# Optimization experiments

Hardware: AMD Instinct MI355X
Metric: run time of the kernel (lower is better)

The kernel has to match this reference:

```python
import jax, jax.numpy as jnp
import numpy as np

N = 50000
E = 1000000
FN = 16
FE = 8
H = 64
DH = 64
LN_EPS = 1e-5


def _layernorm(x, g, b):
    mu = jnp.mean(x, axis=-1, keepdims=True)
    var = jnp.var(x, axis=-1, keepdims=True)
    return (x - mu) * jax.lax.rsqrt(var + LN_EPS) * g + b


def setup_inputs() -> dict:
    key = jax.random.key(0)
    ks = jax.random.split(key, 24)

    def w(k, i, o):
        return jax.random.normal(k, (i, o), jnp.float32) / np.sqrt(i).astype(np.float32)

    inp = {}
    inp["x"] = jax.random.normal(ks[0], (N, FN), jnp.float32)
    inp["edge_index"] = jax.random.randint(ks[1], (2, E), 0, N, dtype=jnp.int32)
    inp["edge_attr"] = jax.random.normal(ks[2], (E, FE), jnp.float32)
    # layer 0 (in_dim = FN, residual is a Linear since FN != H)
    inp["l0_lin_w"] = w(ks[3], FE, FN); inp["l0_lin_b"] = jnp.zeros((FN,), jnp.float32)
    inp["l0_w1"] = w(ks[4], FN, H);    inp["l0_b1"] = jnp.zeros((H,), jnp.float32)
    inp["l0_w2"] = w(ks[5], H, H);     inp["l0_b2"] = jnp.zeros((H,), jnp.float32)
    inp["l0_ln_g"] = jnp.ones((H,), jnp.float32); inp["l0_ln_b"] = jnp.zeros((H,), jnp.float32)
    inp["l0_res_w"] = w(ks[6], FN, H); inp["l0_res_b"] = jnp.zeros((H,), jnp.float32)
    # layers 1, 2 (in_dim = H, residual = identity)
    for li, base in ((1, 7), (2, 11)):
        inp[f"l{li}_lin_w"] = w(ks[base], FE, H);   inp[f"l{li}_lin_b"] = jnp.zeros((H,), jnp.float32)
        inp[f"l{li}_w1"] = w(ks[base + 1], H, H);   inp[f"l{li}_b1"] = jnp.zeros((H,), jnp.float32)
        inp[f"l{li}_w2"] = w(ks[base + 2], H, H);   inp[f"l{li}_b2"] = jnp.zeros((H,), jnp.float32)
        inp[f"l{li}_ln_g"] = jnp.ones((H,), jnp.float32)
        inp[f"l{li}_ln_b"] = jnp.zeros((H,), jnp.float32)
    D_IN = 4 * H + FE
    inp["dec_w1"] = w(ks[20], D_IN, DH);    inp["dec_b1"] = jnp.zeros((DH,), jnp.float32)
    inp["dec_w2"] = w(ks[21], DH, DH // 2); inp["dec_b2"] = jnp.zeros((DH // 2,), jnp.float32)
    inp["dec_w3"] = w(ks[22], DH // 2, 1);  inp["dec_b3"] = jnp.zeros((1,), jnp.float32)
    return inp


def _block(x, src, dst, edge_attr, lin_w, lin_b, w1, b1, w2, b2, ln_g, ln_b, res):
    # GINEConv: message = ReLU(x_src + Lin(edge_attr)); sum-aggregate at dst; eps=0
    msg = jax.nn.relu(x[src] + edge_attr @ lin_w + lin_b)      # (E, D_in)
    aggr = jax.ops.segment_sum(msg, dst, num_segments=N)       # (N, D_in)
    h = jax.nn.relu((x + aggr) @ w1 + b1) @ w2 + b2            # GIN nn MLP -> (N, H)
    h = jax.nn.relu(h)                                         # dropout inactive (eval)
    return _layernorm(h + res, ln_g, ln_b)


def reference(x, edge_index, edge_attr,
              l0_lin_w, l0_lin_b, l0_w1, l0_b1, l0_w2, l0_b2, l0_ln_g, l0_ln_b, l0_res_w, l0_res_b,
              l1_lin_w, l1_lin_b, l1_w1, l1_b1, l1_w2, l1_b2, l1_ln_g, l1_ln_b,
              l2_lin_w, l2_lin_b, l2_w1, l2_b1, l2_w2, l2_b2, l2_ln_g, l2_ln_b,
              dec_w1, dec_b1, dec_w2, dec_b2, dec_w3, dec_b3):
    src, dst = edge_index[0], edge_index[1]
    h = _block(x, src, dst, edge_attr, l0_lin_w, l0_lin_b, l0_w1, l0_b1, l0_w2, l0_b2,
               l0_ln_g, l0_ln_b, x @ l0_res_w + l0_res_b)
    h = _block(h, src, dst, edge_attr, l1_lin_w, l1_lin_b, l1_w1, l1_b1, l1_w2, l1_b2,
               l1_ln_g, l1_ln_b, h)
    h = _block(h, src, dst, edge_attr, l2_lin_w, l2_lin_b, l2_w1, l2_b1, l2_w2, l2_b2,
               l2_ln_g, l2_ln_b, h)
    hs, hd = h[src], h[dst]                                    # (E, H) each
    z = jnp.concatenate([hs, hd, jnp.abs(hs - hd), hs * hd, edge_attr], axis=-1)  # (E, 4H+FE)
    z = jax.nn.relu(z @ dec_w1 + dec_b1)
    z = jax.nn.relu(z @ dec_w2 + dec_b2)
    return (z @ dec_w3 + dec_b3)[:, 0]                         # (E,)
```

## Files before the change

kernel.cpp:

```cpp
#include <hip/hip_runtime.h>

#define NN 50000
#define NE 1000000

constexpr float LN_EPS = 1e-5f;

typedef short bf16x8 __attribute__((ext_vector_type(8)));
typedef float f32x4 __attribute__((ext_vector_type(4)));
typedef uint uvec4 __attribute__((ext_vector_type(4)));
typedef uint uvec2 __attribute__((ext_vector_type(2)));

__device__ inline uint cvtpk(float a, float b) {
  uint r;
  asm("v_cvt_pk_bf16_f32 %0, %1, %2" : "=v"(r) : "v"(a), "v"(b));
  return r;
}
__device__ inline ushort cvt1(float a) {
  uint r;
  asm("v_cvt_pk_bf16_f32 %0, %1, %1" : "=v"(r) : "v"(a));
  return (ushort)r;
}
__device__ inline float bflo(uint u) { union { uint x; float f; } v; v.x = u << 16; return v.f; }
__device__ inline float bfhi(uint u) { union { uint x; float f; } v; v.x = u & 0xffff0000u; return v.f; }

__global__ __launch_bounds__(256) void hist_kernel(const int* __restrict__ ei,
                                                   int* __restrict__ cnt) {
  int e = blockIdx.x * 256 + threadIdx.x;
  if (e < NE) atomicAdd(&cnt[ei[NE + e]], 1);
}

__global__ __launch_bounds__(256) void scan1_kernel(const int* __restrict__ cnt,
                                                    int* __restrict__ off,
                                                    int* __restrict__ bsum) {
  __shared__ int sh[256];
  int t = threadIdx.x;
  int idx = blockIdx.x * 256 + t;
  int v = (idx < NN) ? cnt[idx] : 0;
  sh[t] = v;
  __syncthreads();
  for (int o = 1; o < 256; o <<= 1) {
    int xv = (t >= o) ? sh[t - o] : 0;
    __syncthreads();
    sh[t] += xv;
    __syncthreads();
  }
  if (idx <= NN) off[idx] = sh[t] - v;
  if (t == 255) bsum[blockIdx.x] = sh[255];
}

__global__ __launch_bounds__(256) void scan2_kernel(int* __restrict__ bsum, int nb) {
  __shared__ int sh[256];
  int t = threadIdx.x;
  int v = (t < nb) ? bsum[t] : 0;
  sh[t] = v;
  __syncthreads();
  for (int o = 1; o < 256; o <<= 1) {
    int xv = (t >= o) ? sh[t - o] : 0;
    __syncthreads();
    sh[t] += xv;
    __syncthreads();
  }
  if (t < nb) bsum[t] = sh[t] - v;
}

__global__ __launch_bounds__(256) void scan3_kernel(int* __restrict__ off,
                                                    const int* __restrict__ bsum,
                                                    int* __restrict__ cnt) {
  int idx = blockIdx.x * 256 + threadIdx.x;
  if (idx <= NN) off[idx] += bsum[blockIdx.x];
  if (idx < NN) cnt[idx] = 0;
}

__global__ __launch_bounds__(256) void scatter_kernel(
    const int* __restrict__ ei, const float* __restrict__ ea,
    const int* __restrict__ off, int* __restrict__ cur,
    int* __restrict__ ipos, int* __restrict__ srcp, int* __restrict__ dstp,
    ushort* __restrict__ eapb) {
  int e = blockIdx.x * 256 + threadIdx.x;
  if (e < NE) {
    int d = ei[NE + e];
    int s = ei[e];
    int p = off[d] + atomicAdd(&cur[d], 1);
    ipos[e] = p;
    srcp[p] = s;
    dstp[p] = d;
    const float* eaf = ea + (size_t)e * 8;
    f32x4 e0 = *(const f32x4*)(eaf);
    f32x4 e1 = *(const f32x4*)(eaf + 4);
    uvec4 u;
    u.x = cvtpk(e0.x, e0.y);
    u.y = cvtpk(e0.z, e0.w);
    u.z = cvtpk(e1.x, e1.y);
    u.w = cvtpk(e1.z, e1.w);
    __builtin_nontemporal_store(u, (uvec4*)(eapb + (size_t)p * 8));
  }
}

__global__ __launch_bounds__(256) void unperm_kernel(const float* __restrict__ tmp,
                                                     const int* __restrict__ ipos,
                                                     float* __restrict__ out) {
  int e = blockIdx.x * 256 + threadIdx.x;
  if (e < NE) out[e] = tmp[ipos[e]];
}

__device__ inline float lane_layernorm(float r, float g, float b) {
  float s = r;
#pragma unroll
  for (int m = 32; m >= 1; m >>= 1) s += __shfl_xor(s, m);
  float mu = s * (1.f / 64.f);
  float dv = r - mu;
  float v = dv * dv;
#pragma unroll
  for (int m = 32; m >= 1; m >>= 1) v += __shfl_xor(v, m);
  float var = v * (1.f / 64.f);
  return dv * rsqrtf(var + LN_EPS) * g + b;
}

__global__ __launch_bounds__(256) void layer0_fused(
    const float* __restrict__ x, float* __restrict__ hout,
    ushort* __restrict__ houtbf,
    const ushort* __restrict__ eapb, const int* __restrict__ srcp,
    const int* __restrict__ off,
    const float* __restrict__ lw, const float* __restrict__ lb,
    const float* __restrict__ w1, const float* __restrict__ b1,
    const float* __restrict__ w2, const float* __restrict__ b2,
    const float* __restrict__ lng, const float* __restrict__ lnb,
    const float* __restrict__ rw, const float* __restrict__ rb) {
  int n = blockIdx.x * 4 + (threadIdx.x >> 6);
  int j = threadIdx.x & 63;
  int d = j & 15, slot = j >> 4;
  int start = off[n], end = off[n + 1];
  float lwv[8];
#pragma unroll
  for (int i = 0; i < 8; i++) lwv[i] = lw[i * 16 + d];
  float lbv = lb[d];
  float acc = 0.f;
  for (int base = start; base < end; base += 64) {
    int idx = base + j;
    int sl = (idx < end) ? srcp[idx] : 0;
    int c = min(end - base, 64);
    for (int i0 = 0; i0 < c; i0 += 4) {
      int i = i0 + slot;
      bool valid = i < c;
      int ii = i & 63;
      int s = __shfl(sl, ii);
      int pp = min(base + i0 + slot, NE - 1);
      float ev = bflo((uint)eapb[(size_t)pp * 8 + (d & 7)]);
      float xs = x[(size_t)s * 16 + d];
      float m = lbv + xs;
#pragma unroll
      for (int q = 0; q < 8; q++) m = fmaf(__shfl(ev, slot * 16 + q), lwv[q], m);
      m = fmaxf(m, 0.f);
      acc += valid ? m : 0.f;
    }
  }
  acc += __shfl_xor(acc, 16);
  acc += __shfl_xor(acc, 32);
  float xr = x[(size_t)n * 16 + d];
  float t = xr + acc;
  float q1 = b1[j];
#pragma unroll 4
  for (int k = 0; k < 16; k++) q1 = fmaf(__shfl(t, k), w1[k * 64 + j], q1);
  q1 = fmaxf(q1, 0.f);
  float h2 = b2[j];
  for (int k = 0; k < 64; k++) h2 = fmaf(__shfl(q1, k), w2[k * 64 + j], h2);
  h2 = fmaxf(h2, 0.f);
  float res = rb[j];
#pragma unroll 4
  for (int k = 0; k < 16; k++) res = fmaf(__shfl(xr, k), rw[k * 64 + j], res);
  float v = lane_layernorm(h2 + res, lng[j], lnb[j]);
  hout[(size_t)n * 64 + j] = v;
  houtbf[(size_t)n * 64 + j] = cvt1(v);
}

__device__ inline float edge8_msg(const ushort* __restrict__ hinb, int s, int j,
                                  uint ulo, uint uhi, uint vlo, uint vhi,
                                  const float* lwv, float lbv) {
  float hc = bflo((uint)hinb[(size_t)s * 64 + j]);
  float m = lbv + hc;
  m = fmaf(bflo(ulo), lwv[0], m);
  m = fmaf(bfhi(ulo), lwv[1], m);
  m = fmaf(bflo(uhi), lwv[2], m);
  m = fmaf(bfhi(uhi), lwv[3], m);
  m = fmaf(bflo(vlo), lwv[4], m);
  m = fmaf(bfhi(vlo), lwv[5], m);
  m = fmaf(bflo(vhi), lwv[6], m);
  m = fmaf(bfhi(vhi), lwv[7], m);
  return fmaxf(m, 0.f);
}

__global__ __launch_bounds__(256) void layer_fused(
    const ushort* __restrict__ hinb, const float* __restrict__ hinf,
    float* __restrict__ houtf, ushort* __restrict__ houtbf,
    const ushort* __restrict__ eapb, const int* __restrict__ srcp,
    const int* __restrict__ off,
    const float* __restrict__ lw, const float* __restrict__ lb,
    const float* __restrict__ w1, const float* __restrict__ b1,
    const float* __restrict__ w2, const float* __restrict__ b2,
    const float* __restrict__ lng, const float* __restrict__ lnb) {
  int n = blockIdx.x * 4 + (threadIdx.x >> 6);
  int j = threadIdx.x & 63;
  int start = __builtin_amdgcn_readfirstlane(off[n]);
  int end = __builtin_amdgcn_readfirstlane(off[n + 1]);
  float lwv[8];
#pragma unroll
  for (int i = 0; i < 8; i++) lwv[i] = lw[i * 64 + j];
  float lbv = lb[j];
  float acc = 0.f;
  int p = start;
  for (; p + 8 <= end; p += 8) {
    const uvec4* ip = (const uvec4*)(srcp + p);
    uvec4 I0 = __builtin_nontemporal_load(ip + 0);
    uvec4 I1 = __builtin_nontemporal_load(ip + 1);
    int s0 = __builtin_amdgcn_readfirstlane((int)I0.x);
    int s1 = __builtin_amdgcn_readfirstlane((int)I0.y);
    int s2 = __builtin_amdgcn_readfirstlane((int)I0.z);
    int s3 = __builtin_amdgcn_readfirstlane((int)I0.w);
    int s4 = __builtin_amdgcn_readfirstlane((int)I1.x);
    int s5 = __builtin_amdgcn_readfirstlane((int)I1.y);
    int s6 = __builtin_amdgcn_readfirstlane((int)I1.z);
    int s7 = __builtin_amdgcn_readfirstlane((int)I1.w);
    const uvec4* ep = (const uvec4*)(eapb + (size_t)p * 8);
    uint ua[8][4];
#pragma unroll
    for (int i = 0; i < 8; i++) {
      uvec4 E = __builtin_nontemporal_load(ep + i);
      ua[i][0] = __builtin_amdgcn_readfirstlane(E.x);
      ua[i][1] = __builtin_amdgcn_readfirstlane(E.y);
      ua[i][2] = __builtin_amdgcn_readfirstlane(E.z);
      ua[i][3] = __builtin_amdgcn_readfirstlane(E.w);
    }
    acc += edge8_msg(hinb, s0, j, ua[0][0], ua[0][1], ua[0][2], ua[0][3], lwv, lbv);
    acc += edge8_msg(hinb, s1, j, ua[1][0], ua[1][1], ua[1][2], ua[1][3], lwv, lbv);
    acc += edge8_msg(hinb, s2, j, ua[2][0], ua[2][1], ua[2][2], ua[2][3], lwv, lbv);
    acc += edge8_msg(hinb, s3, j, ua[3][0], ua[3][1], ua[3][2], ua[3][3], lwv, lbv);
    acc += edge8_msg(hinb, s4, j, ua[4][0], ua[4][1], ua[4][2], ua[4][3], lwv, lbv);
    acc += edge8_msg(hinb, s5, j, ua[5][0], ua[5][1], ua[5][2], ua[5][3], lwv, lbv);
    acc += edge8_msg(hinb, s6, j, ua[6][0], ua[6][1], ua[6][2], ua[6][3], lwv, lbv);
    acc += edge8_msg(hinb, s7, j, ua[7][0], ua[7][1], ua[7][2], ua[7][3], lwv, lbv);
  }
  for (; p < end; p++) {
    int s = __builtin_amdgcn_readfirstlane(srcp[p]);
    uvec4 E = __builtin_nontemporal_load((const uvec4*)(eapb + (size_t)p * 8));
    uint e0 = __builtin_amdgcn_readfirstlane(E.x);
    uint e1 = __builtin_amdgcn_readfirstlane(E.y);
    uint e2 = __builtin_amdgcn_readfirstlane(E.z);
    uint e3 = __builtin_amdgcn_readfirstlane(E.w);
    acc += edge8_msg(hinb, s, j, e0, e1, e2, e3, lwv, lbv);
  }
  float hv = __builtin_nontemporal_load(&hinf[(size_t)n * 64 + j]);
  float t = hv + acc;
  float q1 = b1[j];
  for (int k = 0; k < 64; k++) q1 = fmaf(__shfl(t, k), w1[k * 64 + j], q1);
  q1 = fmaxf(q1, 0.f);
  float h2 = b2[j];
  for (int k = 0; k < 64; k++) h2 = fmaf(__shfl(q1, k), w2[k * 64 + j], h2);
  h2 = fmaxf(h2, 0.f);
  float v = lane_layernorm(h2 + hv, lng[j], lnb[j]);
  if (houtf) houtf[(size_t)n * 64 + j] = v;
  houtbf[(size_t)n * 64 + j] = cvt1(v);
}

__global__ __launch_bounds__(256) void prep_kernel(
    const float* __restrict__ w1, const float* __restrict__ w2,
    ushort* __restrict__ w1f, ushort* __restrict__ w2f) {
  int t = blockIdx.x * 256 + threadIdx.x;
  if (t < 18432) {
    int j = t & 7, lane = (t >> 3) & 63, f = t >> 9;
    int k = (f >> 2) * 32 + ((lane >> 4) * 8) + j;
    int n = (f & 3) * 16 + (lane & 15);
    float v = (k < 264) ? w1[k * 64 + n] : 0.f;
    w1f[t] = cvt1(v);
  } else {
    int t2 = t - 18432;
    int j = t2 & 7, lane = (t2 >> 3) & 63, f = t2 >> 9;
    int k = (f >> 1) * 32 + ((lane >> 4) * 8) + j;
    int n = (f & 1) * 16 + (lane & 15);
    w2f[t2] = cvt1(w2[k * 32 + n]);
  }
}

#define YS 72
#define NGRP 31250
#define NBLK 15625
#define BPX 1954

__device__ inline ushort* zsw(ushort* Z, int row, int bo) {
  return (ushort*)((char*)Z + (((row << 9) + bo) ^ ((row & 7) << 4)));
}

__global__ __launch_bounds__(128, 2) void decoder_kernel(
    const ushort* __restrict__ hb,
    const int* __restrict__ srcp, const int* __restrict__ dstp,
    const ushort* __restrict__ eapb,
    const ushort* __restrict__ w1f, const ushort* __restrict__ w2f,
    const float* __restrict__ b1, const float* __restrict__ b2,
    const float* __restrict__ w3, const float* __restrict__ b3,
    float* __restrict__ tmp) {
  __shared__ ushort zbuf[2][32 * 256];
  const int w = threadIdx.x >> 6, l = threadIdx.x & 63;
  const int sub = l & 15, quad = l >> 4;
  int bb = (blockIdx.x & 7) * BPX + (blockIdx.x >> 3);
  if (bb >= NBLK) return;
  const int g = bb * 2 + w;
  ushort* Z = zbuf[w];
  ushort* Y = Z;

  int s32 = __builtin_nontemporal_load(&srcp[g * 32 + (l & 31)]);
  int d32 = __builtin_nontemporal_load(&dstp[g * 32 + (l & 31)]);
  uvec2 pa[8], pb[8];
#pragma unroll
  for (int i = 0; i < 8; i++) {
    int e = 4 * i + quad;
    int s = __shfl(s32, e), d = __shfl(d32, e);
    pa[i] = *(const uvec2*)&hb[(size_t)s * 64 + sub * 4];
    pb[i] = *(const uvec2*)&hb[(size_t)d * 64 + sub * 4];
  }
  bf16x8 eaA = (bf16x8){0, 0, 0, 0, 0, 0, 0, 0};
  bf16x8 eaB = (bf16x8){0, 0, 0, 0, 0, 0, 0, 0};
  if (quad == 0) {
    eaA = *(const bf16x8*)&eapb[((size_t)g * 32 + sub) * 8];
    eaB = *(const bf16x8*)&eapb[((size_t)g * 32 + 16 + sub) * 8];
  }

  float b1v[4];
#pragma unroll
  for (int t = 0; t < 4; t++) b1v[t] = b1[t * 16 + sub];
  float b2v0 = b2[sub], b2v1 = b2[16 + sub];
  float w3v0 = w3[sub], w3v1 = w3[16 + sub];
  float b3v = b3[0];

#pragma unroll
  for (int i = 0; i < 8; i++) {
    int e = 4 * i + quad;
    uvec2 a = pa[i], b = pb[i];
    *(uvec2*)zsw(Z, e, sub * 8) = a;
    *(uvec2*)zsw(Z, e, 128 + sub * 8) = b;
    float a0 = bflo(a.x), a1 = bfhi(a.x), a2 = bflo(a.y), a3 = bfhi(a.y);
    float c0 = bflo(b.x), c1 = bfhi(b.x), c2 = bflo(b.y), c3 = bfhi(b.y);
    uvec2 u;
    u.x = cvtpk(fabsf(a0 - c0), fabsf(a1 - c1));
    u.y = cvtpk(fabsf(a2 - c2), fabsf(a3 - c3));
    *(uvec2*)zsw(Z, e, 256 + sub * 8) = u;
    u.x = cvtpk(a0 * c0, a1 * c1);
    u.y = cvtpk(a2 * c2, a3 * c3);
    *(uvec2*)zsw(Z, e, 384 + sub * 8) = u;
  }

  f32x4 acc[2][4];
#pragma unroll
  for (int m = 0; m < 2; m++)
#pragma unroll
    for (int t = 0; t < 4; t++) acc[m][t] = (f32x4){0.f, 0.f, 0.f, 0.f};
#pragma unroll
  for (int s = 0; s < 8; s++) {
    bf16x8 afA = *(const bf16x8*)zsw(Z, sub, s * 64 + quad * 16);
    bf16x8 afB = *(const bf16x8*)zsw(Z, 16 + sub, s * 64 + quad * 16);
#pragma unroll
    for (int t = 0; t < 4; t++) {
      bf16x8 bf = ((const bf16x8*)w1f)[(s * 4 + t) * 64 + l];
      acc[0][t] = __builtin_amdgcn_mfma_f32_16x16x32_bf16(afA, bf, acc[0][t], 0, 0, 0);
      acc[1][t] = __builtin_amdgcn_mfma_f32_16x16x32_bf16(afB, bf, acc[1][t], 0, 0, 0);
    }
  }
#pragma unroll
  for (int t = 0; t < 4; t++) {
    bf16x8 bf = ((const bf16x8*)w1f)[(32 + t) * 64 + l];
    acc[0][t] = __builtin_amdgcn_mfma_f32_16x16x32_bf16(eaA, bf, acc[0][t], 0, 0, 0);
    acc[1][t] = __builtin_amdgcn_mfma_f32_16x16x32_bf16(eaB, bf, acc[1][t], 0, 0, 0);
  }
#pragma unroll
  for (int m = 0; m < 2; m++)
#pragma unroll
    for (int t = 0; t < 4; t++)
#pragma unroll
      for (int r = 0; r < 4; r++)
        Y[(m * 16 + quad * 4 + r) * YS + t * 16 + sub] =
            cvt1(fmaxf(acc[m][t][r] + b1v[t], 0.f));

  bf16x8 w2frag[4];
#pragma unroll
  for (int f = 0; f < 4; f++) w2frag[f] = ((const bf16x8*)w2f)[f * 64 + l];
  f32x4 acc2[2][2];
#pragma unroll
  for (int m = 0; m < 2; m++) {
    acc2[m][0] = (f32x4){0.f, 0.f, 0.f, 0.f};
    acc2[m][1] = (f32x4){0.f, 0.f, 0.f, 0.f};
#pragma unroll
    for (int ks = 0; ks < 2; ks++) {
      union { bf16x8 v; ushort4 u[2]; } ya;
      int o = (m * 16 + sub) * YS + ks * 32 + quad * 8;
      ya.u[0] = *(const ushort4*)&Y[o];
      ya.u[1] = *(const ushort4*)&Y[o + 4];
      acc2[m][0] = __builtin_amdgcn_mfma_f32_16x16x32_bf16(ya.v, w2frag[ks * 2 + 0],
                                                           acc2[m][0], 0, 0, 0);
      acc2[m][1] = __builtin_amdgcn_mfma_f32_16x16x32_bf16(ya.v, w2frag[ks * 2 + 1],
                                                           acc2[m][1], 0, 0, 0);
    }
  }
#pragma unroll
  for (int m = 0; m < 2; m++)
#pragma unroll
    for (int r = 0; r < 4; r++) {
      float o = fmaxf(acc2[m][0][r] + b2v0, 0.f) * w3v0 +
                fmaxf(acc2[m][1][r] + b2v1, 0.f) * w3v1;
      o += __shfl_xor(o, 1);
      o += __shfl_xor(o, 2);
      o += __shfl_xor(o, 4);
      o += __shfl_xor(o, 8);
      if (sub == 0) tmp[g * 32 + m * 16 + quad * 4 + r] = o + b3v;
    }
}

extern "C" void kernel_launch(void* const* d_in, const int* in_sizes, int n_in,
                              void* d_out, int out_size, void* d_ws, size_t ws_size,
                              hipStream_t stream) {
  const float* x = (const float*)d_in[0];
  const int* ei = (const int*)d_in[1];
  const float* ea = (const float*)d_in[2];
  const float* l0_lin_w = (const float*)d_in[3];
  const float* l0_lin_b = (const float*)d_in[4];
  const float* l0_w1 = (const float*)d_in[5];
  const float* l0_b1 = (const float*)d_in[6];
  const float* l0_w2 = (const float*)d_in[7];
  const float* l0_b2 = (const float*)d_in[8];
  const float* l0_ln_g = (const float*)d_in[9];
  const float* l0_ln_b = (const float*)d_in[10];
  const float* l0_res_w = (const float*)d_in[11];
  const float* l0_res_b = (const float*)d_in[12];
  const float* dec_w1 = (const float*)d_in[29];
  const float* dec_b1 = (const float*)d_in[30];
  const float* dec_w2 = (const float*)d_in[31];
  const float* dec_b2 = (const float*)d_in[32];
  const float* dec_w3 = (const float*)d_in[33];
  const float* dec_b3 = (const float*)d_in[34];

  float* h_a = (float*)d_ws;
  float* h_b = h_a + (size_t)NN * 64;
  ushort* hbA = (ushort*)(h_b + (size_t)NN * 64);
  ushort* hbB = hbA + (size_t)NN * 64;
  int* ipos = (int*)(hbB + (size_t)NN * 64);
  int* srcp = ipos + NE;
  int* dstp = srcp + NE;
  float* tmp = (float*)(dstp + NE);
  int* off = (int*)(tmp + NE);
  int* cnt = off + (NN + 1);
  int* bsum = cnt + NN;
  ushort* w1f = (ushort*)(bsum + 256);
  ushort* w2f = w1f + 18432;
  ushort* eapb = w2f + 2048;

  const int EB = (NE + 255) / 256;
  const int SB = (NN + 256) / 256;

  hipMemsetAsync(cnt, 0, (size_t)NN * sizeof(int), stream);
  hist_kernel<<<EB, 256, 0, stream>>>(ei, cnt);
  scan1_kernel<<<SB, 256, 0, stream>>>(cnt, off, bsum);
  scan2_kernel<<<1, 256, 0, stream>>>(bsum, SB);
  scan3_kernel<<<SB, 256, 0, stream>>>(off, bsum, cnt);
  scatter_kernel<<<EB, 256, 0, stream>>>(ei, ea, off, cnt, ipos, srcp, dstp, eapb);

  layer0_fused<<<NN / 4, 256, 0, stream>>>(x, h_a, hbA, eapb, srcp, off,
                                           l0_lin_w, l0_lin_b, l0_w1, l0_b1,
                                           l0_w2, l0_b2, l0_ln_g, l0_ln_b,
                                           l0_res_w, l0_res_b);
  layer_fused<<<NN / 4, 256, 0, stream>>>(hbA, h_a, h_b, hbB, eapb, srcp, off,
                                          (const float*)d_in[13], (const float*)d_in[14],
                                          (const float*)d_in[15], (const float*)d_in[16],
                                          (const float*)d_in[17], (const float*)d_in[18],
                                          (const float*)d_in[19], (const float*)d_in[20]);
  layer_fused<<<NN / 4, 256, 0, stream>>>(hbB, h_b, (float*)nullptr, hbA, eapb, srcp, off,
                                          (const float*)d_in[21], (const float*)d_in[22],
                                          (const float*)d_in[23], (const float*)d_in[24],
                                          (const float*)d_in[25], (const float*)d_in[26],
                                          (const float*)d_in[27], (const float*)d_in[28]);

  prep_kernel<<<80, 256, 0, stream>>>(dec_w1, dec_w2, w1f, w2f);
  decoder_kernel<<<8 * BPX, 128, 0, stream>>>(hbA, srcp, dstp, eapb,
                                              w1f, w2f, dec_b1, dec_b2,
                                              dec_w3, dec_b3, tmp);
  unperm_kernel<<<EB, 256, 0, stream>>>(tmp, ipos, (float*)d_out);
}
```

Baseline: 641.5 us.

## Load decoder MFMA A-fragments directly from gathered rows, drop LDS staging

The decoder previously gathered node embeddings into a swizzled 32x256 LDS tile, built the |a-b| and a*b features there, and then read MFMA A-fragments back from it. It now gathers each edge's src/dst rows straight into the MFMA A-fragment register layout (two 8-element chunks per lane) and computes the abs-diff and product fragments in registers. The K blocks are reordered to match, which removes the LDS writes and reads for the first layer. LDS shrinks to the small Y buffer, so launch bounds rise to 4 blocks per SM, and the Y read becomes a single 16-byte load. Register pressure grows, which could limit the extra occupancy.

```diff
diff --git a/kernel.cpp b/kernel.cpp
--- a/kernel.cpp
+++ b/kernel.cpp
@@ -281,15 +281,23 @@
 }
 
 #define YS 72
-#define NGRP 31250
 #define NBLK 15625
 #define BPX 1954
 
-__device__ inline ushort* zsw(ushort* Z, int row, int bo) {
-  return (ushort*)((char*)Z + (((row << 9) + bo) ^ ((row & 7) << 4)));
-}
-
-__global__ __launch_bounds__(128, 2) void decoder_kernel(
+__device__ inline void absmul(bf16x8 a, bf16x8 b, bf16x8& dd, bf16x8& pp) {
+  union U { bf16x8 v; uvec4 u; } ua, ub, ud, up;
+  ua.v = a; ub.v = b;
+#pragma unroll
+  for (int i = 0; i < 4; i++) {
+    float a0 = bflo(ua.u[i]), a1 = bfhi(ua.u[i]);
+    float b0 = bflo(ub.u[i]), b1 = bfhi(ub.u[i]);
+    ud.u[i] = cvtpk(fabsf(a0 - b0), fabsf(a1 - b1));
+    up.u[i] = cvtpk(a0 * b0, a1 * b1);
+  }
+  dd = ud.v; pp = up.v;
+}
+
+__global__ __launch_bounds__(128, 4) void decoder_kernel(
     const ushort* __restrict__ hb,
     const int* __restrict__ srcp, const int* __restrict__ dstp,
     const ushort* __restrict__ eapb,
@@ -297,30 +305,34 @@
     const float* __restrict__ b1, const float* __restrict__ b2,
     const float* __restrict__ w3, const float* __restrict__ b3,
     float* __restrict__ tmp) {
-  __shared__ ushort zbuf[2][32 * 256];
+  __shared__ ushort ybuf[2][32 * YS];
   const int w = threadIdx.x >> 6, l = threadIdx.x & 63;
   const int sub = l & 15, quad = l >> 4;
   int bb = (blockIdx.x & 7) * BPX + (blockIdx.x >> 3);
   if (bb >= NBLK) return;
   const int g = bb * 2 + w;
-  ushort* Z = zbuf[w];
-  ushort* Y = Z;
+  ushort* Y = ybuf[w];
 
   int s32 = __builtin_nontemporal_load(&srcp[g * 32 + (l & 31)]);
   int d32 = __builtin_nontemporal_load(&dstp[g * 32 + (l & 31)]);
-  uvec2 pa[8], pb[8];
-#pragma unroll
-  for (int i = 0; i < 8; i++) {
-    int e = 4 * i + quad;
-    int s = __shfl(s32, e), d = __shfl(d32, e);
-    pa[i] = *(const uvec2*)&hb[(size_t)s * 64 + sub * 4];
-    pb[i] = *(const uvec2*)&hb[(size_t)d * 64 + sub * 4];
-  }
-  bf16x8 eaA = (bf16x8){0, 0, 0, 0, 0, 0, 0, 0};
-  bf16x8 eaB = (bf16x8){0, 0, 0, 0, 0, 0, 0, 0};
+
+  bf16x8 alo[2], ahi[2], blo[2], bhi[2];
+#pragma unroll
+  for (int m = 0; m < 2; m++) {
+    int sA = __shfl(s32, m * 16 + sub);
+    int dA = __shfl(d32, m * 16 + sub);
+    const ushort* pa = hb + (size_t)sA * 64 + quad * 8;
+    const ushort* pb = hb + (size_t)dA * 64 + quad * 8;
+    alo[m] = *(const bf16x8*)pa;
+    ahi[m] = *(const bf16x8*)(pa + 32);
+    blo[m] = *(const bf16x8*)pb;
+    bhi[m] = *(const bf16x8*)(pb + 32);
+  }
+  bf16x8 eaf0 = (bf16x8){0, 0, 0, 0, 0, 0, 0, 0};
+  bf16x8 eaf1 = (bf16x8){0, 0, 0, 0, 0, 0, 0, 0};
   if (quad == 0) {
-    eaA = *(const bf16x8*)&eapb[((size_t)g * 32 + sub) * 8];
-    eaB = *(const bf16x8*)&eapb[((size_t)g * 32 + 16 + sub) * 8];
+    eaf0 = *(const bf16x8*)&eapb[((size_t)g * 32 + sub) * 8];
+    eaf1 = *(const bf16x8*)&eapb[((size_t)g * 32 + 16 + sub) * 8];
   }
 
   float b1v[4];
@@ -330,45 +342,44 @@
   float w3v0 = w3[sub], w3v1 = w3[16 + sub];
   float b3v = b3[0];
 
-#pragma unroll
-  for (int i = 0; i < 8; i++) {
-    int e = 4 * i + quad;
-    uvec2 a = pa[i], b = pb[i];
-    *(uvec2*)zsw(Z, e, sub * 8) = a;
-    *(uvec2*)zsw(Z, e, 128 + sub * 8) = b;
-    float a0 = bflo(a.x), a1 = bfhi(a.x), a2 = bflo(a.y), a3 = bfhi(a.y);
-    float c0 = bflo(b.x), c1 = bfhi(b.x), c2 = bflo(b.y), c3 = bfhi(b.y);
-    uvec2 u;
-    u.x = cvtpk(fabsf(a0 - c0), fabsf(a1 - c1));
-    u.y = cvtpk(fabsf(a2 - c2), fabsf(a3 - c3));
-    *(uvec2*)zsw(Z, e, 256 + sub * 8) = u;
-    u.x = cvtpk(a0 * c0, a1 * c1);
-    u.y = cvtpk(a2 * c2, a3 * c3);
-    *(uvec2*)zsw(Z, e, 384 + sub * 8) = u;
-  }
-
   f32x4 acc[2][4];
 #pragma unroll
   for (int m = 0; m < 2; m++)
 #pragma unroll
     for (int t = 0; t < 4; t++) acc[m][t] = (f32x4){0.f, 0.f, 0.f, 0.f};
-#pragma unroll
-  for (int s = 0; s < 8; s++) {
-    bf16x8 afA = *(const bf16x8*)zsw(Z, sub, s * 64 + quad * 16);
-    bf16x8 afB = *(const bf16x8*)zsw(Z, 16 + sub, s * 64 + quad * 16);
-#pragma unroll
-    for (int t = 0; t < 4; t++) {
-      bf16x8 bf = ((const bf16x8*)w1f)[(s * 4 + t) * 64 + l];
-      acc[0][t] = __builtin_amdgcn_mfma_f32_16x16x32_bf16(afA, bf, acc[0][t], 0, 0, 0);
-      acc[1][t] = __builtin_amdgcn_mfma_f32_16x16x32_bf16(afB, bf, acc[1][t], 0, 0, 0);
-    }
-  }
-#pragma unroll
-  for (int t = 0; t < 4; t++) {
-    bf16x8 bf = ((const bf16x8*)w1f)[(32 + t) * 64 + l];
-    acc[0][t] = __builtin_amdgcn_mfma_f32_16x16x32_bf16(eaA, bf, acc[0][t], 0, 0, 0);
-    acc[1][t] = __builtin_amdgcn_mfma_f32_16x16x32_bf16(eaB, bf, acc[1][t], 0, 0, 0);
-  }
+
+#define MF(sB, f0, f1)                                                        \
+  {                                                                           \
+    _Pragma("unroll") for (int t = 0; t < 4; t++) {                           \
+      bf16x8 bfv = ((const bf16x8*)w1f)[((sB)*4 + t) * 64 + l];               \
+      acc[0][t] = __builtin_amdgcn_mfma_f32_16x16x32_bf16(f0, bfv, acc[0][t], \
+                                                          0, 0, 0);           \
+      acc[1][t] = __builtin_amdgcn_mfma_f32_16x16x32_bf16(f1, bfv, acc[1][t], \
+                                                          0, 0, 0);           \
+    }                                                                         \
+  }
+
+  {
+    bf16x8 dlo0, plo0, dlo1, plo1;
+    absmul(alo[0], blo[0], dlo0, plo0);
+    absmul(alo[1], blo[1], dlo1, plo1);
+    MF(0, alo[0], alo[1]);
+    MF(2, blo[0], blo[1]);
+    MF(4, dlo0, dlo1);
+    MF(6, plo0, plo1);
+  }
+  {
+    bf16x8 dhi0, phi0, dhi1, phi1;
+    absmul(ahi[0], bhi[0], dhi0, phi0);
+    absmul(ahi[1], bhi[1], dhi1, phi1);
+    MF(1, ahi[0], ahi[1]);
+    MF(3, bhi[0], bhi[1]);
+    MF(5, dhi0, dhi1);
+    MF(7, phi0, phi1);
+  }
+  MF(8, eaf0, eaf1);
+#undef MF
+
 #pragma unroll
   for (int m = 0; m < 2; m++)
 #pragma unroll
@@ -388,13 +399,10 @@
     acc2[m][1] = (f32x4){0.f, 0.f, 0.f, 0.f};
 #pragma unroll
     for (int ks = 0; ks < 2; ks++) {
-      union { bf16x8 v; ushort4 u[2]; } ya;
-      int o = (m * 16 + sub) * YS + ks * 32 + quad * 8;
-      ya.u[0] = *(const ushort4*)&Y[o];
-      ya.u[1] = *(const ushort4*)&Y[o + 4];
-      acc2[m][0] = __builtin_amdgcn_mfma_f32_16x16x32_bf16(ya.v, w2frag[ks * 2 + 0],
+      bf16x8 ya = *(const bf16x8*)&Y[(m * 16 + sub) * YS + ks * 32 + quad * 8];
+      acc2[m][0] = __builtin_amdgcn_mfma_f32_16x16x32_bf16(ya, w2frag[ks * 2 + 0],
                                                            acc2[m][0], 0, 0, 0);
-      acc2[m][1] = __builtin_amdgcn_mfma_f32_16x16x32_bf16(ya.v, w2frag[ks * 2 + 1],
+      acc2[m][1] = __builtin_amdgcn_mfma_f32_16x16x32_bf16(ya, w2frag[ks * 2 + 1],
                                                            acc2[m][1], 0, 0, 0);
     }
   }
```

Result: faster. 617.1 us (-3.8%).
